# Optimization experiments

Measured on AMD Instinct MI355X. Metric: run time of the kernel, lower is better.

The kernel has to match this reference:

```python
import jax, jax.numpy as jnp
import numpy as np

N, Lq, Lk, D = 4, 2048, 2048, 1024
H, DH = 16, 64  # n_heads, projection_dim
NEG_INF = jnp.float32(-1e30)


def setup_inputs() -> dict:
    key = jax.random.key(0)
    ks = jax.random.split(key, 6)
    query = jax.random.normal(ks[0], (N, Lq, D), dtype=jnp.float32)
    key_t = jax.random.normal(ks[1], (N, Lk, D), dtype=jnp.float32)
    s = 1.0 / np.sqrt(D)
    Wq = jax.random.normal(ks[2], (D, D), dtype=jnp.float32) * s
    Wk = jax.random.normal(ks[3], (D, D), dtype=jnp.float32) * s
    Wv = jax.random.normal(ks[4], (D, D), dtype=jnp.float32) * s
    # causal mask: True where attention is forbidden (j > i)
    mask = jnp.triu(jnp.ones((Lq, Lk), dtype=bool), k=1)
    # per-sample valid lengths in [1024, 2048); padding at the tail
    valid_len = jax.random.randint(ks[5], (N,), Lk // 2, Lk)
    padding_mask = jnp.arange(Lk)[None, :] >= valid_len[:, None]  # (N, Lk) bool
    return {"query": query, "key": key_t, "Wq": Wq, "Wk": Wk, "Wv": Wv,
            "mask": mask, "padding_mask": padding_mask}


def reference(query, key, Wq, Wk, Wv, mask, padding_mask):
    n, lq, _ = query.shape
    lk = key.shape[1]
    # torch Linear (no bias): x @ W.T ; split heads -> (N, H, L, DH)
    q = (query @ Wq.T).reshape(n, lq, H, DH).transpose(0, 2, 1, 3)
    k = (key @ Wk.T).reshape(n, lk, H, DH).transpose(0, 2, 1, 3)
    v = (key @ Wv.T).reshape(n, lk, H, DH).transpose(0, 2, 1, 3)
    # per-sample scaling: sqrt(number of non-padded keys) (module quirk, not sqrt(d))
    valid = jnp.sum(~padding_mask, axis=-1).astype(query.dtype)  # (N,)
    scaling = jnp.sqrt(valid)[:, None, None, None]
    score = jnp.einsum('nhqd,nhkd->nhqk', q, k) / scaling
    score = jnp.where(mask[None, None, :, :], NEG_INF, score)
    score = jnp.where(padding_mask[:, None, None, :], NEG_INF, score)
    attn = jax.nn.softmax(score, axis=-1)
    out = jnp.einsum('nhqk,nhkd->nhqd', attn, v)
    return out.transpose(0, 2, 1, 3).reshape(n, lq, H * DH)
```

## Files before the change

kernel.cpp:

```cpp
#include <hip/hip_runtime.h>
#include <hip/hip_bf16.h>
#include <math.h>


#define N_S 4
#define LQ 2048
#define LK 2048
#define DM 1024
#define NHEAD 16
#define DHEAD 64

typedef __attribute__((ext_vector_type(8))) short short8;
typedef __attribute__((ext_vector_type(4))) float f32x4;

typedef const __attribute__((address_space(1))) void* gptr_t;
typedef __attribute__((address_space(3))) void* lptr_t;

#define GLOAD_LDS(g, l) \
    __builtin_amdgcn_global_load_lds((gptr_t)(const void*)(g), (lptr_t)(void*)(l), 16, 0, 0)

static __device__ __forceinline__ unsigned int pkbf(float a, float b) {
    __hip_bfloat162 h = __float22bfloat162_rn(make_float2(a, b));
    unsigned int u;
    __builtin_memcpy(&u, &h, 4);
    return u;
}

static __device__ __forceinline__ f32x4 zero4() {
    f32x4 v; v[0] = 0.f; v[1] = 0.f; v[2] = 0.f; v[3] = 0.f; return v;
}

static __device__ __forceinline__ void meta_body(const void* __restrict__ pm,
                                                 int* __restrict__ valid_out,
                                                 float* __restrict__ scale_out) {
    __shared__ int okInt, hasPair, okF32;
    __shared__ int counts[4];
    int t = threadIdx.x;
    if (t == 0) { okInt = 1; hasPair = 0; okF32 = 1; }
    if (t < 4) counts[t] = 0;
    __syncthreads();

    const unsigned int* w = (const unsigned int*)pm;
    int bad_int = 0, pair = 0, bad_f32 = 0;
    for (int i = t; i < 2048; i += 256) {
        unsigned int v = w[i];
        if (v > 1u) bad_int = 1;
        if (v == 0x3F803F80u) pair = 1;
        if (v != 0u && v != 0x3F800000u) bad_f32 = 1;
    }
    if (bad_int) okInt = 0;
    if (pair)    hasPair = 1;
    if (bad_f32) okF32 = 0;
    __syncthreads();

    int mode = okInt ? 0 : (hasPair ? 1 : (okF32 ? 2 : 3));
    for (int n = 0; n < 4; n++) {
        int cnt = 0;
        for (int j = t; j < LK; j += 256) {
            int idx = n * LK + j;
            bool z;
            if (mode == 0)      z = (((const int*)pm)[idx] == 0);
            else if (mode == 1) z = (((const unsigned short*)pm)[idx] == 0);
            else if (mode == 2) z = (w[idx] == 0u);
            else                z = (((const unsigned char*)pm)[idx] == 0);
            cnt += z ? 1 : 0;
        }
        atomicAdd(&counts[n], cnt);
    }
    __syncthreads();
    if (t < 4) {
        int c = counts[t] > 0 ? counts[t] : 1;
        valid_out[t] = c;
        scale_out[t] = 1.0f / sqrtf((float)c);
    }
}

__global__ void meta_kernel(const void* __restrict__ pm,
                            int* __restrict__ valid_out,
                            float* __restrict__ scale_out) {
    meta_body(pm, valid_out, scale_out);
}

static __device__ __forceinline__ void conv16(const float* src,
                                              unsigned short* dst, size_t idx) {
    f32x4 a0 = *(const f32x4*)(src + idx);
    f32x4 a1 = *(const f32x4*)(src + idx + 4);
    f32x4 a2 = *(const f32x4*)(src + idx + 8);
    f32x4 a3 = *(const f32x4*)(src + idx + 12);
    uint4 u0, u1;
    u0.x = pkbf(a0[0], a0[1]); u0.y = pkbf(a0[2], a0[3]);
    u0.z = pkbf(a1[0], a1[1]); u0.w = pkbf(a1[2], a1[3]);
    u1.x = pkbf(a2[0], a2[1]); u1.y = pkbf(a2[2], a2[3]);
    u1.z = pkbf(a3[0], a3[1]); u1.w = pkbf(a3[2], a3[3]);
    *(uint4*)(void*)(dst + idx) = u0;
    *(uint4*)(void*)(dst + idx + 8) = u1;
}

__global__ __launch_bounds__(256) void convw_kernel(
    const float* __restrict__ Wq, const float* __restrict__ Wk,
    const float* __restrict__ Wv,
    unsigned short* __restrict__ Wqb, unsigned short* __restrict__ Wkb,
    unsigned short* __restrict__ Wvb)
{
    int z = blockIdx.y;
    const float* src = (z == 0) ? Wq : ((z == 1) ? Wk : Wv);
    unsigned short* dst = (z == 0) ? Wqb : ((z == 1) ? Wkb : Wvb);
    conv16(src, dst, ((size_t)blockIdx.x * 256 + threadIdx.x) * 16);
}

__global__ __launch_bounds__(256) void convx_kernel(
    const float* __restrict__ src, unsigned short* __restrict__ dst)
{
    conv16(src, dst, ((size_t)blockIdx.x * 256 + threadIdx.x) * 16);
}

__global__ __launch_bounds__(256) void prep_kernel(
    const void* __restrict__ pm, int* __restrict__ valid_out,
    float* __restrict__ scale_out,
    const float* __restrict__ Wq, const float* __restrict__ Wk,
    const float* __restrict__ Wv,
    unsigned short* __restrict__ Wqb, unsigned short* __restrict__ Wkb,
    unsigned short* __restrict__ Wvb,
    const float* __restrict__ xq, const float* __restrict__ xk,
    unsigned short* __restrict__ dq, unsigned short* __restrict__ dk)
{
    int b = blockIdx.x;
    int t = threadIdx.x;
    if (b == 0) {
        meta_body(pm, valid_out, scale_out);
    } else if (b <= 768) {
        int bb = b - 1;
        int z = bb >> 8;
        const float* src = (z == 0) ? Wq : ((z == 1) ? Wk : Wv);
        unsigned short* dst = (z == 0) ? Wqb : ((z == 1) ? Wkb : Wvb);
        conv16(src, dst, ((size_t)(bb & 255) * 256 + t) * 16);
    } else {
        int bb = b - 769;
        const float* src = (bb >= 2048) ? xk : xq;
        unsigned short* dst = (bb >= 2048) ? dk : dq;
        int x = (bb >= 2048) ? bb - 2048 : bb;
        conv16(src, dst, ((size_t)x * 256 + t) * 16);
    }
}

static __device__ __forceinline__ void proj_body(
    const unsigned short* __restrict__ XbQ, const unsigned short* __restrict__ XbK,
    const unsigned short* __restrict__ Wqb, const unsigned short* __restrict__ Wkb,
    const unsigned short* __restrict__ Wvb,
    const float* __restrict__ scal, const int* __restrict__ valid_arr,
    unsigned short* __restrict__ Qb, unsigned short* __restrict__ Kb,
    unsigned short* __restrict__ Vt, int bxi, int byi, int z)
{
    int m0 = bxi << 7, n0 = byi << 7;
    if (z >= 1) {
        int n = m0 >> 11, ml = m0 & 2047;
        int tv64 = ((valid_arr[n] + 63) >> 6) << 6;
        if (ml >= tv64) return;
    }

    const unsigned short* W = (z == 0) ? Wqb : ((z == 1) ? Wkb : Wvb);
    const unsigned short* Xb = (z == 0) ? XbQ : XbK;

    __shared__ unsigned short Xls[128 * 32];
    __shared__ unsigned short Wls[128 * 32];

    int t = threadIdx.x;
    int wave = t >> 6, lane = t & 63;
    int l15 = lane & 15, quad = lane >> 4;
    int wa = wave >> 1, wb = wave & 1;

    int srow = t >> 2;
    int sg = ((t & 3) ^ (srow & 3)) << 3;
    const unsigned short* gX0 = Xb + (size_t)(m0 + srow) * DM + sg;
    const unsigned short* gX1 = Xb + (size_t)(m0 + 64 + srow) * DM + sg;
    const unsigned short* gW0 = W + (size_t)(n0 + srow) * DM + sg;
    const unsigned short* gW1 = W + (size_t)(n0 + 64 + srow) * DM + sg;

    f32x4 acc[4][4];
    #pragma unroll
    for (int i = 0; i < 4; i++)
        #pragma unroll
        for (int j = 0; j < 4; j++) acc[i][j] = zero4();

    int aoff = ((quad ^ (l15 & 3)) << 3);
    const unsigned short* Abuf = (z < 2) ? Wls : Xls;
    const unsigned short* Bbuf = (z < 2) ? Xls : Wls;

    for (int kk = 0; kk < DM; kk += 32) {
        __syncthreads();
        GLOAD_LDS(gX0 + kk, Xls + wave * 512);
        GLOAD_LDS(gX1 + kk, Xls + 2048 + wave * 512);
        GLOAD_LDS(gW0 + kk, Wls + wave * 512);
        GLOAD_LDS(gW1 + kk, Wls + 2048 + wave * 512);
        __syncthreads();

        short8 af[4], bf[4];
        #pragma unroll
        for (int ai = 0; ai < 4; ai++)
            af[ai] = *(const short8*)(const void*)(
                Abuf + ((wa * 64 + ai * 16 + l15) << 5) + aoff);
        #pragma unroll
        for (int bi = 0; bi < 4; bi++)
            bf[bi] = *(const short8*)(const void*)(
                Bbuf + ((wb * 64 + bi * 16 + l15) << 5) + aoff);
        #pragma unroll
        for (int ai = 0; ai < 4; ai++)
            #pragma unroll
            for (int bi = 0; bi < 4; bi++)
                acc[ai][bi] = __builtin_amdgcn_mfma_f32_16x16x32_bf16(
                    af[ai], bf[bi], acc[ai][bi], 0, 0, 0);
    }

    if (z < 2) {
        unsigned short* O = (z == 0) ? Qb : Kb;
        #pragma unroll
        for (int bi = 0; bi < 4; bi++) {
            int token = m0 + wb * 64 + bi * 16 + l15;
            float qs = 1.0f;
            if (z == 0) qs = scal[token >> 11] * 1.44269504f;
            #pragma unroll
            for (int ai = 0; ai < 4; ai++) {
                int feat = n0 + wa * 64 + ai * 16 + quad * 4;
                float v0 = acc[ai][bi][0], v1 = acc[ai][bi][1];
                float v2 = acc[ai][bi][2], v3 = acc[ai][bi][3];
                if (z == 0) { v0 *= qs; v1 *= qs; v2 *= qs; v3 *= qs; }
                uint2 u;
                u.x = pkbf(v0, v1);
                u.y = pkbf(v2, v3);
                *(uint2*)(void*)(O + (size_t)token * DM + feat) = u;
            }
        }
    } else {
        #pragma unroll
        for (int ai = 0; ai < 4; ai++) {
            int token0 = m0 + wa * 64 + ai * 16 + quad * 4;
            int n = token0 >> 11, tl = token0 & 2047;
            #pragma unroll
            for (int bi = 0; bi < 4; bi++) {
                int feat = n0 + wb * 64 + bi * 16 + l15;
                uint2 u;
                u.x = pkbf(acc[ai][bi][0], acc[ai][bi][1]);
                u.y = pkbf(acc[ai][bi][2], acc[ai][bi][3]);
                *(uint2*)(void*)(Vt + ((size_t)n * DM + feat) * LK + tl) = u;
            }
        }
    }
}

__global__ __launch_bounds__(256) void proj_bf16_kernel(
    const unsigned short* __restrict__ XbQ, const unsigned short* __restrict__ XbK,
    const unsigned short* __restrict__ Wqb, const unsigned short* __restrict__ Wkb,
    const unsigned short* __restrict__ Wvb,
    const float* __restrict__ scal, const int* __restrict__ valid_arr,
    unsigned short* __restrict__ Qb, unsigned short* __restrict__ Kb,
    unsigned short* __restrict__ Vt, int zbase)
{
    proj_body(XbQ, XbK, Wqb, Wkb, Wvb, scal, valid_arr, Qb, Kb, Vt,
              blockIdx.x, blockIdx.y, blockIdx.z + zbase);
}

__global__ __launch_bounds__(256) void proj_bf16_swz_kernel(
    const unsigned short* __restrict__ XbQ, const unsigned short* __restrict__ XbK,
    const unsigned short* __restrict__ Wqb, const unsigned short* __restrict__ Wkb,
    const unsigned short* __restrict__ Wvb,
    const float* __restrict__ scal, const int* __restrict__ valid_arr,
    unsigned short* __restrict__ Qb, unsigned short* __restrict__ Kb,
    unsigned short* __restrict__ Vt)
{
    int id = blockIdx.x;
    int s = id >> 3;
    int g = (id & 7) * 24 + (s >> 3);
    int y = s & 7;
    int z = g >> 6, x = g & 63;
    proj_body(XbQ, XbK, Wqb, Wkb, Wvb, scal, valid_arr, Qb, Kb, Vt, x, y, z);
}

__global__ __launch_bounds__(256) void proj_f32_kernel(
    const float* __restrict__ Xq, const float* __restrict__ Xk,
    const unsigned short* __restrict__ Wqb, const unsigned short* __restrict__ Wkb,
    const unsigned short* __restrict__ Wvb,
    const float* __restrict__ scal,
    unsigned short* __restrict__ Qb, unsigned short* __restrict__ Kb,
    unsigned short* __restrict__ Vt)
{
    int z = blockIdx.z;
    const float* X = (z == 0) ? Xq : Xk;
    const unsigned short* W = (z == 0) ? Wqb : ((z == 1) ? Wkb : Wvb);

    __shared__ unsigned short Xls[128 * 32];
    __shared__ unsigned short Wls[128 * 32];

    int t = threadIdx.x;
    int wave = t >> 6, lane = t & 63;
    int l15 = lane & 15, quad = lane >> 4;
    int wa = wave >> 1, wb = wave & 1;
    int m0 = blockIdx.x << 7, n0 = blockIdx.y << 7;

    int arow = t >> 1, ah = t & 1;
    int ag0 = ((2 * ah)     ^ (arow & 3)) << 3;
    int ag1 = ((2 * ah + 1) ^ (arow & 3)) << 3;
    const float* gX = X + (size_t)(m0 + arow) * DM;
    unsigned short* lX = Xls + arow * 32 + ah * 16;

    int brow = t >> 2;
    int bg = ((t & 3) ^ (brow & 3)) << 3;
    const unsigned short* gW0 = W + (size_t)(n0 + brow) * DM + bg;
    const unsigned short* gW1 = W + (size_t)(n0 + 64 + brow) * DM + bg;

    f32x4 acc[4][4];
    #pragma unroll
    for (int i = 0; i < 4; i++)
        #pragma unroll
        for (int j = 0; j < 4; j++) acc[i][j] = zero4();

    int aoff = ((quad ^ (l15 & 3)) << 3);

    f32x4 an0 = *(const f32x4*)(gX + ag0);
    f32x4 an1 = *(const f32x4*)(gX + ag0 + 4);
    f32x4 an2 = *(const f32x4*)(gX + ag1);
    f32x4 an3 = *(const f32x4*)(gX + ag1 + 4);

    const unsigned short* Abuf = (z < 2) ? Wls : Xls;
    const unsigned short* Bbuf = (z < 2) ? Xls : Wls;

    for (int kk = 0; kk < DM; kk += 32) {
        __syncthreads();
        GLOAD_LDS(gW0 + kk, Wls + wave * 512);
        GLOAD_LDS(gW1 + kk, Wls + 2048 + wave * 512);
        uint4 ua, ub;
        ua.x = pkbf(an0[0], an0[1]); ua.y = pkbf(an0[2], an0[3]);
        ua.z = pkbf(an1[0], an1[1]); ua.w = pkbf(an1[2], an1[3]);
        ub.x = pkbf(an2[0], an2[1]); ub.y = pkbf(an2[2], an2[3]);
        ub.z = pkbf(an3[0], an3[1]); ub.w = pkbf(an3[2], an3[3]);
        *(uint4*)(void*)(lX)     = ua;
        *(uint4*)(void*)(lX + 8) = ub;
        __syncthreads();

        if (kk + 32 < DM) {
            an0 = *(const f32x4*)(gX + kk + 32 + ag0);
            an1 = *(const f32x4*)(gX + kk + 32 + ag0 + 4);
            an2 = *(const f32x4*)(gX + kk + 32 + ag1);
            an3 = *(const f32x4*)(gX + kk + 32 + ag1 + 4);
        }

        short8 af[4], bf[4];
        #pragma unroll
        for (int ai = 0; ai < 4; ai++)
            af[ai] = *(const short8*)(const void*)(
                Abuf + ((wa * 64 + ai * 16 + l15) << 5) + aoff);
        #pragma unroll
        for (int bi = 0; bi < 4; bi++)
            bf[bi] = *(const short8*)(const void*)(
                Bbuf + ((wb * 64 + bi * 16 + l15) << 5) + aoff);
        #pragma unroll
        for (int ai = 0; ai < 4; ai++)
            #pragma unroll
            for (int bi = 0; bi < 4; bi++)
                acc[ai][bi] = __builtin_amdgcn_mfma_f32_16x16x32_bf16(
                    af[ai], bf[bi], acc[ai][bi], 0, 0, 0);
    }

    if (z < 2) {
        unsigned short* O = (z == 0) ? Qb : Kb;
        #pragma unroll
        for (int bi = 0; bi < 4; bi++) {
            int token = m0 + wb * 64 + bi * 16 + l15;
            float qs = 1.0f;
            if (z == 0) qs = scal[token >> 11] * 1.44269504f;
            #pragma unroll
            for (int ai = 0; ai < 4; ai++) {
                int feat = n0 + wa * 64 + ai * 16 + quad * 4;
                float v0 = acc[ai][bi][0], v1 = acc[ai][bi][1];
                float v2 = acc[ai][bi][2], v3 = acc[ai][bi][3];
                if (z == 0) { v0 *= qs; v1 *= qs; v2 *= qs; v3 *= qs; }
                uint2 u;
                u.x = pkbf(v0, v1);
                u.y = pkbf(v2, v3);
                *(uint2*)(void*)(O + (size_t)token * DM + feat) = u;
            }
        }
    } else {
        #pragma unroll
        for (int ai = 0; ai < 4; ai++) {
            int token0 = m0 + wa * 64 + ai * 16 + quad * 4;
            int n = token0 >> 11, tl = token0 & 2047;
            #pragma unroll
            for (int bi = 0; bi < 4; bi++) {
                int feat = n0 + wb * 64 + bi * 16 + l15;
                uint2 u;
                u.x = pkbf(acc[ai][bi][0], acc[ai][bi][1]);
                u.y = pkbf(acc[ai][bi][2], acc[ai][bi][3]);
                *(uint2*)(void*)(Vt + ((size_t)n * DM + feat) * LK + tl) = u;
            }
        }
    }
}

__global__ __launch_bounds__(256) void attn_kernel(
    const unsigned short* __restrict__ Qb, const unsigned short* __restrict__ Kb,
    const unsigned short* __restrict__ Vt,
    const int* __restrict__ valid_arr,
    float* __restrict__ out)
{
    __shared__ unsigned short Kls[3][64 * 64];

    int id = blockIdx.x;
    int slot = id >> 3;
    int nh = (id & 7) * 8 + (slot >> 4);
    int bx = slot & 15;

    int n = nh >> 4, h = nh & 15;
    int tA = bx, tB = 31 - bx;

    int valid = valid_arr[n];
    int tvalid = (valid + 63) >> 6;
    int TlA = (tA + 1 < tvalid) ? tA + 1 : tvalid;
    int TlB = (tB + 1 < tvalid) ? tB + 1 : tvalid;

    int t = threadIdx.x;
    int wave = t >> 6, lane = t & 63;
    int l15 = lane & 15, quad = lane >> 4;

    int qyA = tA * 64 + wave * 16 + l15;
    int qyB = tB * 64 + wave * 16 + l15;
    int qw0A = tA * 64 + wave * 16;
    int qw0B = tB * 64 + wave * 16;

    const unsigned short* QrowA = Qb + ((size_t)n * LQ + qyA) * DM + h * DHEAD;
    const unsigned short* QrowB = Qb + ((size_t)n * LQ + qyB) * DM + h * DHEAD;
    short8 qfA0 = *(const short8*)(const void*)(QrowA + quad * 8);
    short8 qfA1 = *(const short8*)(const void*)(QrowA + 32 + quad * 8);
    short8 qfB0 = *(const short8*)(const void*)(QrowB + quad * 8);
    short8 qfB1 = *(const short8*)(const void*)(QrowB + 32 + quad * 8);

    f32x4 OA[4], OB[4];
    #pragma unroll
    for (int i = 0; i < 4; i++) { OA[i] = zero4(); OB[i] = zero4(); }
    f32x4 LAcc = zero4(), LBcc = zero4();

    short8 onesf;
    #pragma unroll
    for (int i = 0; i < 8; i++) onesf[i] = (short)0x3F80;

    const unsigned short* Kbase = Kb + (size_t)n * LK * DM + h * DHEAD;
    const unsigned short* Vbase = Vt + ((size_t)n * DM + h * DHEAD) * LK;

    int srow0 = t >> 3;
    int sgk   = (((t & 7) ^ (srow0 & 7)) << 3);

    GLOAD_LDS(Kbase + (size_t)srow0 * DM + sgk,        &Kls[0][0] + wave * 512);
    GLOAD_LDS(Kbase + (size_t)(32 + srow0) * DM + sgk, &Kls[0][0] + 2048 + wave * 512);
    if (TlB > 1) {
        GLOAD_LDS(Kbase + (size_t)(64 + srow0) * DM + sgk,
                  &Kls[1][0] + wave * 512);
        GLOAD_LDS(Kbase + (size_t)(96 + srow0) * DM + sgk,
                  &Kls[1][0] + 2048 + wave * 512);
        asm volatile("s_waitcnt vmcnt(2)" ::: "memory");
    } else {
        asm volatile("s_waitcnt vmcnt(0)" ::: "memory");
    }

    int cur = 0;
    for (int kt = 0; kt < TlB; kt++) {
        int jb = kt << 6;
        bool doA = (kt < TlA);
        int nxt = (cur == 0) ? 2 : cur - 1;

        __builtin_amdgcn_sched_barrier(0);
        __builtin_amdgcn_s_barrier();
        __builtin_amdgcn_sched_barrier(0);

        short8 vf0[4], vf1[4];
        #pragma unroll
        for (int cb = 0; cb < 4; cb++) {
            vf0[cb] = *(const short8*)(const void*)(
                Vbase + (size_t)(cb * 16 + l15) * LK + jb + quad * 8);
            vf1[cb] = *(const short8*)(const void*)(
                Vbase + (size_t)(cb * 16 + l15) * LK + jb + 32 + quad * 8);
        }

        f32x4 sA[4], sB[4];
        __builtin_amdgcn_s_setprio(1);
        #pragma unroll
        for (int cb = 0; cb < 4; cb++) {
            const unsigned short* krow = &Kls[cur][0] + ((cb * 16 + l15) << 6);
            short8 kf0 = *(const short8*)(const void*)(krow + ((quad ^ (l15 & 7)) << 3));
            short8 kf1 = *(const short8*)(const void*)(krow + (((4 + quad) ^ (l15 & 7)) << 3));
            f32x4 sb = zero4();
            sb = __builtin_amdgcn_mfma_f32_16x16x32_bf16(kf0, qfB0, sb, 0, 0, 0);
            sb = __builtin_amdgcn_mfma_f32_16x16x32_bf16(kf1, qfB1, sb, 0, 0, 0);
            sB[cb] = sb;
            if (doA) {
                f32x4 sa = zero4();
                sa = __builtin_amdgcn_mfma_f32_16x16x32_bf16(kf0, qfA0, sa, 0, 0, 0);
                sa = __builtin_amdgcn_mfma_f32_16x16x32_bf16(kf1, qfA1, sa, 0, 0, 0);
                sA[cb] = sa;
            }
        }
        __builtin_amdgcn_s_setprio(0);

        if (kt + 2 < TlB) {
            int jb2 = jb + 128;
            GLOAD_LDS(Kbase + (size_t)(jb2 + srow0) * DM + sgk,
                      &Kls[nxt][0] + wave * 512);
            GLOAD_LDS(Kbase + (size_t)(jb2 + 32 + srow0) * DM + sgk,
                      &Kls[nxt][0] + 2048 + wave * 512);
        }

        if (jb + 63 > qw0B || jb + 64 > valid) {
            #pragma unroll
            for (int cb = 0; cb < 4; cb++) {
                int jb2 = jb + cb * 16 + quad * 4;
                #pragma unroll
                for (int r = 0; r < 4; r++) {
                    int j = jb2 + r;
                    if (j > qyB || j >= valid) sB[cb][r] = -1e30f;
                }
            }
        }
        short8 pfB0, pfB1;
        {
            unsigned int lo[4], hi[4];
            #pragma unroll
            for (int cb = 0; cb < 4; cb++) {
                lo[cb] = pkbf(__builtin_amdgcn_exp2f(sB[cb][0]),
                              __builtin_amdgcn_exp2f(sB[cb][1]));
                hi[cb] = pkbf(__builtin_amdgcn_exp2f(sB[cb][2]),
                              __builtin_amdgcn_exp2f(sB[cb][3]));
            }
            asm("v_permlane32_swap_b32 %0, %1" : "+v"(lo[0]), "+v"(lo[1]));
            asm("v_permlane32_swap_b32 %0, %1" : "+v"(hi[0]), "+v"(hi[1]));
            asm("v_permlane32_swap_b32 %0, %1" : "+v"(lo[2]), "+v"(lo[3]));
            asm("v_permlane32_swap_b32 %0, %1" : "+v"(hi[2]), "+v"(hi[3]));
            asm("v_permlane16_swap_b32 %0, %1" : "+v"(lo[0]), "+v"(lo[1]));
            asm("v_permlane16_swap_b32 %0, %1" : "+v"(hi[0]), "+v"(hi[1]));
            asm("v_permlane16_swap_b32 %0, %1" : "+v"(lo[2]), "+v"(lo[3]));
            asm("v_permlane16_swap_b32 %0, %1" : "+v"(hi[2]), "+v"(hi[3]));
            uint4 w0, w1;
            w0.x = lo[0]; w0.y = hi[0]; w0.z = lo[1]; w0.w = hi[1];
            w1.x = lo[2]; w1.y = hi[2]; w1.z = lo[3]; w1.w = hi[3];
            __builtin_memcpy(&pfB0, &w0, 16);
            __builtin_memcpy(&pfB1, &w1, 16);
        }

        __builtin_amdgcn_s_setprio(1);
        #pragma unroll
        for (int cb = 0; cb < 4; cb++) {
            OB[cb] = __builtin_amdgcn_mfma_f32_16x16x32_bf16(pfB0, vf0[cb], OB[cb], 0, 0, 0);
            OB[cb] = __builtin_amdgcn_mfma_f32_16x16x32_bf16(pfB1, vf1[cb], OB[cb], 0, 0, 0);
        }
        LBcc = __builtin_amdgcn_mfma_f32_16x16x32_bf16(pfB0, onesf, LBcc, 0, 0, 0);
        LBcc = __builtin_amdgcn_mfma_f32_16x16x32_bf16(pfB1, onesf, LBcc, 0, 0, 0);
        __builtin_amdgcn_s_setprio(0);

        if (doA) {
            if (jb + 63 > qw0A || jb + 64 > valid) {
                #pragma unroll
                for (int cb = 0; cb < 4; cb++) {
                    int jb2 = jb + cb * 16 + quad * 4;
                    #pragma unroll
                    for (int r = 0; r < 4; r++) {
                        int j = jb2 + r;
                        if (j > qyA || j >= valid) sA[cb][r] = -1e30f;
                    }
                }
            }
            short8 pfA0, pfA1;
            {
                unsigned int lo[4], hi[4];
                #pragma unroll
                for (int cb = 0; cb < 4; cb++) {
                    lo[cb] = pkbf(__builtin_amdgcn_exp2f(sA[cb][0]),
                                  __builtin_amdgcn_exp2f(sA[cb][1]));
                    hi[cb] = pkbf(__builtin_amdgcn_exp2f(sA[cb][2]),
                                  __builtin_amdgcn_exp2f(sA[cb][3]));
                }
                asm("v_permlane32_swap_b32 %0, %1" : "+v"(lo[0]), "+v"(lo[1]));
                asm("v_permlane32_swap_b32 %0, %1" : "+v"(hi[0]), "+v"(hi[1]));
                asm("v_permlane32_swap_b32 %0, %1" : "+v"(lo[2]), "+v"(lo[3]));
                asm("v_permlane32_swap_b32 %0, %1" : "+v"(hi[2]), "+v"(hi[3]));
                asm("v_permlane16_swap_b32 %0, %1" : "+v"(lo[0]), "+v"(lo[1]));
                asm("v_permlane16_swap_b32 %0, %1" : "+v"(hi[0]), "+v"(hi[1]));
                asm("v_permlane16_swap_b32 %0, %1" : "+v"(lo[2]), "+v"(lo[3]));
                asm("v_permlane16_swap_b32 %0, %1" : "+v"(hi[2]), "+v"(hi[3]));
                uint4 w0, w1;
                w0.x = lo[0]; w0.y = hi[0]; w0.z = lo[1]; w0.w = hi[1];
                w1.x = lo[2]; w1.y = hi[2]; w1.z = lo[3]; w1.w = hi[3];
                __builtin_memcpy(&pfA0, &w0, 16);
                __builtin_memcpy(&pfA1, &w1, 16);
            }
            __builtin_amdgcn_s_setprio(1);
            #pragma unroll
            for (int cb = 0; cb < 4; cb++) {
                OA[cb] = __builtin_amdgcn_mfma_f32_16x16x32_bf16(pfA0, vf0[cb], OA[cb], 0, 0, 0);
                OA[cb] = __builtin_amdgcn_mfma_f32_16x16x32_bf16(pfA1, vf1[cb], OA[cb], 0, 0, 0);
            }
            LAcc = __builtin_amdgcn_mfma_f32_16x16x32_bf16(pfA0, onesf, LAcc, 0, 0, 0);
            LAcc = __builtin_amdgcn_mfma_f32_16x16x32_bf16(pfA1, onesf, LAcc, 0, 0, 0);
            __builtin_amdgcn_s_setprio(0);
        }

        cur = (cur == 2) ? 0 : cur + 1;
    }

    float* obase = out + ((size_t)n * LQ) * DM + h * DHEAD;
    #pragma unroll
    for (int r = 0; r < 4; r++) {
        float iA = 1.0f / LAcc[r];
        float iB = 1.0f / LBcc[r];
        int rowA = tA * 64 + wave * 16 + quad * 4 + r;
        int rowB = tB * 64 + wave * 16 + quad * 4 + r;
        #pragma unroll
        for (int cb = 0; cb < 4; cb++) {
            obase[(size_t)rowA * DM + cb * 16 + l15] = OA[cb][r] * iA;
            obase[(size_t)rowB * DM + cb * 16 + l15] = OB[cb][r] * iB;
        }
    }
}

extern "C" void kernel_launch(void* const* d_in, const int* in_sizes, int n_in,
                              void* d_out, int out_size, void* d_ws, size_t ws_size,
                              hipStream_t stream)
{
    (void)in_sizes; (void)n_in; (void)out_size;

    const float* query = (const float*)d_in[0];
    const float* key   = (const float*)d_in[1];
    const float* Wq    = (const float*)d_in[2];
    const float* Wk    = (const float*)d_in[3];
    const float* Wv    = (const float*)d_in[4];
    const void* pmask  = d_in[6];

    char* ws = (char*)d_ws;
    unsigned short* Qb  = (unsigned short*)(ws);
    unsigned short* Kb  = (unsigned short*)(ws + (size_t)16 * 1024 * 1024);
    unsigned short* Vt  = (unsigned short*)(ws + (size_t)32 * 1024 * 1024);
    int*   valid = (int*)  (ws + (size_t)48 * 1024 * 1024);
    float* scal  = (float*)(ws + (size_t)48 * 1024 * 1024 + 64);
    unsigned short* Wqb = (unsigned short*)(ws + (size_t)48 * 1024 * 1024 + 4096);
    unsigned short* Wkb = Wqb + (size_t)DM * DM;
    unsigned short* Wvb = Wkb + (size_t)DM * DM;
    unsigned short* XbQ = Wvb + (size_t)DM * DM;
    unsigned short* XbK = XbQ + (size_t)N_S * LQ * DM;

    size_t xbytes      = (size_t)N_S * LQ * DM * 2;
    size_t need_phased = (size_t)(48 * 1024 * 1024) + 4096
                       + 3 * (size_t)DM * DM * 2 + xbytes;
    size_t need_full   = need_phased + xbytes;

    if (ws_size >= need_full) {
        prep_kernel<<<dim3(1 + 768 + 4096), 256, 0, stream>>>(
            pmask, valid, scal, Wq, Wk, Wv, Wqb, Wkb, Wvb,
            query, key, XbQ, XbK);
        proj_bf16_swz_kernel<<<dim3(1536), 256, 0, stream>>>(
            XbQ, XbK, Wqb, Wkb, Wvb, scal, valid, Qb, Kb, Vt);
    } else if (ws_size >= need_phased) {
        meta_kernel<<<1, 256, 0, stream>>>(pmask, valid, scal);
        convw_kernel<<<dim3(256, 3), 256, 0, stream>>>(Wq, Wk, Wv, Wqb, Wkb, Wvb);
        convx_kernel<<<2048, 256, 0, stream>>>(query, XbQ);
        proj_bf16_kernel<<<dim3(64, 8, 1), 256, 0, stream>>>(
            XbQ, XbQ, Wqb, Wkb, Wvb, scal, valid, Qb, Kb, Vt, 0);
        convx_kernel<<<2048, 256, 0, stream>>>(key, XbQ);
        proj_bf16_kernel<<<dim3(64, 8, 2), 256, 0, stream>>>(
            XbQ, XbQ, Wqb, Wkb, Wvb, scal, valid, Qb, Kb, Vt, 1);
    } else {
        meta_kernel<<<1, 256, 0, stream>>>(pmask, valid, scal);
        convw_kernel<<<dim3(256, 3), 256, 0, stream>>>(Wq, Wk, Wv, Wqb, Wkb, Wvb);
        proj_f32_kernel<<<dim3(64, 8, 3), 256, 0, stream>>>(
            query, key, Wqb, Wkb, Wvb, scal, Qb, Kb, Vt);
    }

    attn_kernel<<<dim3(1024), 256, 0, stream>>>(Qb, Kb, Vt, valid,
                                                (float*)d_out);
}
```

Baseline: 334.2 us.

## Split paired causal query tiles into one tile per block, doubling grid

The attention kernel previously had each block handle two complementary query tiles (tA and 31-tA) that share K/V loads, which balanced causal work. Now each block handles a single 64-row query tile, and the grid is doubled to 2048 blocks. Blocks are remapped so heads are grouped per XCD and longer tiles are scheduled first. This cuts per-block register pressure and may raise occupancy, at the cost of loading K/V separately for each tile and giving blocks unequal amounts of work.

```diff
diff --git a/kernel.cpp b/kernel.cpp
--- a/kernel.cpp
+++ b/kernel.cpp
@@ -405,38 +405,32 @@
     __shared__ unsigned short Kls[3][64 * 64];
 
     int id = blockIdx.x;
+    int xcd = id & 7;
     int slot = id >> 3;
-    int nh = (id & 7) * 8 + (slot >> 4);
-    int bx = slot & 15;
-
-    int n = nh >> 4, h = nh & 15;
-    int tA = bx, tB = 31 - bx;
+    int g = slot >> 5;
+    int tQ = 31 - (slot & 31);
+    int n = g >> 1;
+    int h = 2 * xcd + (g & 1);
 
     int valid = valid_arr[n];
     int tvalid = (valid + 63) >> 6;
-    int TlA = (tA + 1 < tvalid) ? tA + 1 : tvalid;
-    int TlB = (tB + 1 < tvalid) ? tB + 1 : tvalid;
+    int Tl = (tQ + 1 < tvalid) ? tQ + 1 : tvalid;
 
     int t = threadIdx.x;
     int wave = t >> 6, lane = t & 63;
     int l15 = lane & 15, quad = lane >> 4;
 
-    int qyA = tA * 64 + wave * 16 + l15;
-    int qyB = tB * 64 + wave * 16 + l15;
-    int qw0A = tA * 64 + wave * 16;
-    int qw0B = tB * 64 + wave * 16;
-
-    const unsigned short* QrowA = Qb + ((size_t)n * LQ + qyA) * DM + h * DHEAD;
-    const unsigned short* QrowB = Qb + ((size_t)n * LQ + qyB) * DM + h * DHEAD;
-    short8 qfA0 = *(const short8*)(const void*)(QrowA + quad * 8);
-    short8 qfA1 = *(const short8*)(const void*)(QrowA + 32 + quad * 8);
-    short8 qfB0 = *(const short8*)(const void*)(QrowB + quad * 8);
-    short8 qfB1 = *(const short8*)(const void*)(QrowB + 32 + quad * 8);
-
-    f32x4 OA[4], OB[4];
+    int qy = tQ * 64 + wave * 16 + l15;
+    int qw0 = tQ * 64 + wave * 16;
+
+    const unsigned short* Qrow = Qb + ((size_t)n * LQ + qy) * DM + h * DHEAD;
+    short8 qf0 = *(const short8*)(const void*)(Qrow + quad * 8);
+    short8 qf1 = *(const short8*)(const void*)(Qrow + 32 + quad * 8);
+
+    f32x4 O[4];
     #pragma unroll
-    for (int i = 0; i < 4; i++) { OA[i] = zero4(); OB[i] = zero4(); }
-    f32x4 LAcc = zero4(), LBcc = zero4();
+    for (int i = 0; i < 4; i++) O[i] = zero4();
+    f32x4 Lc = zero4();
 
     short8 onesf;
     #pragma unroll
@@ -450,7 +444,7 @@
 
     GLOAD_LDS(Kbase + (size_t)srow0 * DM + sgk,        &Kls[0][0] + wave * 512);
     GLOAD_LDS(Kbase + (size_t)(32 + srow0) * DM + sgk, &Kls[0][0] + 2048 + wave * 512);
-    if (TlB > 1) {
+    if (Tl > 1) {
         GLOAD_LDS(Kbase + (size_t)(64 + srow0) * DM + sgk,
                   &Kls[1][0] + wave * 512);
         GLOAD_LDS(Kbase + (size_t)(96 + srow0) * DM + sgk,
@@ -461,9 +455,8 @@
     }
 
     int cur = 0;
-    for (int kt = 0; kt < TlB; kt++) {
+    for (int kt = 0; kt < Tl; kt++) {
         int jb = kt << 6;
-        bool doA = (kt < TlA);
         int nxt = (cur == 0) ? 2 : cur - 1;
 
         __builtin_amdgcn_sched_barrier(0);
@@ -479,27 +472,21 @@
                 Vbase + (size_t)(cb * 16 + l15) * LK + jb + 32 + quad * 8);
         }
 
-        f32x4 sA[4], sB[4];
+        f32x4 s[4];
         __builtin_amdgcn_s_setprio(1);
         #pragma unroll
         for (int cb = 0; cb < 4; cb++) {
             const unsigned short* krow = &Kls[cur][0] + ((cb * 16 + l15) << 6);
             short8 kf0 = *(const short8*)(const void*)(krow + ((quad ^ (l15 & 7)) << 3));
             short8 kf1 = *(const short8*)(const void*)(krow + (((4 + quad) ^ (l15 & 7)) << 3));
-            f32x4 sb = zero4();
-            sb = __builtin_amdgcn_mfma_f32_16x16x32_bf16(kf0, qfB0, sb, 0, 0, 0);
-            sb = __builtin_amdgcn_mfma_f32_16x16x32_bf16(kf1, qfB1, sb, 0, 0, 0);
-            sB[cb] = sb;
-            if (doA) {
-                f32x4 sa = zero4();
-                sa = __builtin_amdgcn_mfma_f32_16x16x32_bf16(kf0, qfA0, sa, 0, 0, 0);
-                sa = __builtin_amdgcn_mfma_f32_16x16x32_bf16(kf1, qfA1, sa, 0, 0, 0);
-                sA[cb] = sa;
-            }
+            f32x4 sv = zero4();
+            sv = __builtin_amdgcn_mfma_f32_16x16x32_bf16(kf0, qf0, sv, 0, 0, 0);
+            sv = __builtin_amdgcn_mfma_f32_16x16x32_bf16(kf1, qf1, sv, 0, 0, 0);
+            s[cb] = sv;
         }
         __builtin_amdgcn_s_setprio(0);
 
-        if (kt + 2 < TlB) {
+        if (kt + 2 < Tl) {
             int jb2 = jb + 128;
             GLOAD_LDS(Kbase + (size_t)(jb2 + srow0) * DM + sgk,
                       &Kls[nxt][0] + wave * 512);
@@ -507,26 +494,26 @@
                       &Kls[nxt][0] + 2048 + wave * 512);
         }
 
-        if (jb + 63 > qw0B || jb + 64 > valid) {
+        if (jb + 63 > qw0 || jb + 64 > valid) {
             #pragma unroll
             for (int cb = 0; cb < 4; cb++) {
                 int jb2 = jb + cb * 16 + quad * 4;
                 #pragma unroll
                 for (int r = 0; r < 4; r++) {
                     int j = jb2 + r;
-                    if (j > qyB || j >= valid) sB[cb][r] = -1e30f;
+                    if (j > qy || j >= valid) s[cb][r] = -1e30f;
                 }
             }
         }
-        short8 pfB0, pfB1;
+        short8 pf0, pf1;
         {
             unsigned int lo[4], hi[4];
             #pragma unroll
             for (int cb = 0; cb < 4; cb++) {
-                lo[cb] = pkbf(__builtin_amdgcn_exp2f(sB[cb][0]),
-                              __builtin_amdgcn_exp2f(sB[cb][1]));
-                hi[cb] = pkbf(__builtin_amdgcn_exp2f(sB[cb][2]),
-                              __builtin_amdgcn_exp2f(sB[cb][3]));
+                lo[cb] = pkbf(__builtin_amdgcn_exp2f(s[cb][0]),
+                              __builtin_amdgcn_exp2f(s[cb][1]));
+                hi[cb] = pkbf(__builtin_amdgcn_exp2f(s[cb][2]),
+                              __builtin_amdgcn_exp2f(s[cb][3]));
             }
             asm("v_permlane32_swap_b32 %0, %1" : "+v"(lo[0]), "+v"(lo[1]));
             asm("v_permlane32_swap_b32 %0, %1" : "+v"(hi[0]), "+v"(hi[1]));
@@ -539,66 +526,19 @@
             uint4 w0, w1;
             w0.x = lo[0]; w0.y = hi[0]; w0.z = lo[1]; w0.w = hi[1];
             w1.x = lo[2]; w1.y = hi[2]; w1.z = lo[3]; w1.w = hi[3];
-            __builtin_memcpy(&pfB0, &w0, 16);
-            __builtin_memcpy(&pfB1, &w1, 16);
+            __builtin_memcpy(&pf0, &w0, 16);
+            __builtin_memcpy(&pf1, &w1, 16);
         }
 
         __builtin_amdgcn_s_setprio(1);
         #pragma unroll
         for (int cb = 0; cb < 4; cb++) {
-            OB[cb] = __builtin_amdgcn_mfma_f32_16x16x32_bf16(pfB0, vf0[cb], OB[cb], 0, 0, 0);
-            OB[cb] = __builtin_amdgcn_mfma_f32_16x16x32_bf16(pfB1, vf1[cb], OB[cb], 0, 0, 0);
-        }
-        LBcc = __builtin_amdgcn_mfma_f32_16x16x32_bf16(pfB0, onesf, LBcc, 0, 0, 0);
-        LBcc = __builtin_amdgcn_mfma_f32_16x16x32_bf16(pfB1, onesf, LBcc, 0, 0, 0);
+            O[cb] = __builtin_amdgcn_mfma_f32_16x16x32_bf16(pf0, vf0[cb], O[cb], 0, 0, 0);
+            O[cb] = __builtin_amdgcn_mfma_f32_16x16x32_bf16(pf1, vf1[cb], O[cb], 0, 0, 0);
+        }
+        Lc = __builtin_amdgcn_mfma_f32_16x16x32_bf16(pf0, onesf, Lc, 0, 0, 0);
+        Lc = __builtin_amdgcn_mfma_f32_16x16x32_bf16(pf1, onesf, Lc, 0, 0, 0);
         __builtin_amdgcn_s_setprio(0);
-
-        if (doA) {
-            if (jb + 63 > qw0A || jb + 64 > valid) {
-                #pragma unroll
-                for (int cb = 0; cb < 4; cb++) {
-                    int jb2 = jb + cb * 16 + quad * 4;
-                    #pragma unroll
-                    for (int r = 0; r < 4; r++) {
-                        int j = jb2 + r;
-                        if (j > qyA || j >= valid) sA[cb][r] = -1e30f;
-                    }
-                }
-            }
-            short8 pfA0, pfA1;
-            {
-                unsigned int lo[4], hi[4];
-                #pragma unroll
-                for (int cb = 0; cb < 4; cb++) {
-                    lo[cb] = pkbf(__builtin_amdgcn_exp2f(sA[cb][0]),
-                                  __builtin_amdgcn_exp2f(sA[cb][1]));
-                    hi[cb] = pkbf(__builtin_amdgcn_exp2f(sA[cb][2]),
-                                  __builtin_amdgcn_exp2f(sA[cb][3]));
-                }
-                asm("v_permlane32_swap_b32 %0, %1" : "+v"(lo[0]), "+v"(lo[1]));
-                asm("v_permlane32_swap_b32 %0, %1" : "+v"(hi[0]), "+v"(hi[1]));
-                asm("v_permlane32_swap_b32 %0, %1" : "+v"(lo[2]), "+v"(lo[3]));
-                asm("v_permlane32_swap_b32 %0, %1" : "+v"(hi[2]), "+v"(hi[3]));
-                asm("v_permlane16_swap_b32 %0, %1" : "+v"(lo[0]), "+v"(lo[1]));
-                asm("v_permlane16_swap_b32 %0, %1" : "+v"(hi[0]), "+v"(hi[1]));
-                asm("v_permlane16_swap_b32 %0, %1" : "+v"(lo[2]), "+v"(lo[3]));
-                asm("v_permlane16_swap_b32 %0, %1" : "+v"(hi[2]), "+v"(hi[3]));
-                uint4 w0, w1;
-                w0.x = lo[0]; w0.y = hi[0]; w0.z = lo[1]; w0.w = hi[1];
-                w1.x = lo[2]; w1.y = hi[2]; w1.z = lo[3]; w1.w = hi[3];
-                __builtin_memcpy(&pfA0, &w0, 16);
-                __builtin_memcpy(&pfA1, &w1, 16);
-            }
-            __builtin_amdgcn_s_setprio(1);
-            #pragma unroll
-            for (int cb = 0; cb < 4; cb++) {
-                OA[cb] = __builtin_amdgcn_mfma_f32_16x16x32_bf16(pfA0, vf0[cb], OA[cb], 0, 0, 0);
-                OA[cb] = __builtin_amdgcn_mfma_f32_16x16x32_bf16(pfA1, vf1[cb], OA[cb], 0, 0, 0);
-            }
-            LAcc = __builtin_amdgcn_mfma_f32_16x16x32_bf16(pfA0, onesf, LAcc, 0, 0, 0);
-            LAcc = __builtin_amdgcn_mfma_f32_16x16x32_bf16(pfA1, onesf, LAcc, 0, 0, 0);
-            __builtin_amdgcn_s_setprio(0);
-        }
 
         cur = (cur == 2) ? 0 : cur + 1;
     }
@@ -606,14 +546,11 @@
     float* obase = out + ((size_t)n * LQ) * DM + h * DHEAD;
     #pragma unroll
     for (int r = 0; r < 4; r++) {
-        float iA = 1.0f / LAcc[r];
-        float iB = 1.0f / LBcc[r];
-        int rowA = tA * 64 + wave * 16 + quad * 4 + r;
-        int rowB = tB * 64 + wave * 16 + quad * 4 + r;
+        float iL = 1.0f / Lc[r];
+        int row = tQ * 64 + wave * 16 + quad * 4 + r;
         #pragma unroll
         for (int cb = 0; cb < 4; cb++) {
-            obase[(size_t)rowA * DM + cb * 16 + l15] = OA[cb][r] * iA;
-            obase[(size_t)rowB * DM + cb * 16 + l15] = OB[cb][r] * iB;
+            obase[(size_t)row * DM + cb * 16 + l15] = O[cb][r] * iL;
         }
     }
 }
@@ -670,6 +607,6 @@
             query, key, Wqb, Wkb, Wvb, scal, Qb, Kb, Vt);
     }
 
-    attn_kernel<<<dim3(1024), 256, 0, stream>>>(Qb, Kb, Vt, valid,
+    attn_kernel<<<dim3(2048), 256, 0, stream>>>(Qb, Kb, Vt, valid,
                                                 (float*)d_out);
 }
```

After: 363.3 us. 8.7% more time.

## Share K tiles across two query-tile pairs in 512-thread attention blocks

Applied to the files above, without the earlier changes.

The attention kernel now uses 512-thread blocks. Each block handles four query tiles of one (batch, head): two balanced causal pairs, one per group of four waves. Every K tile staged in LDS is therefore reused by twice as many waves, halving the number of blocks and the K global-to-LDS traffic per query tile. The head-to-XCD mapping is also regrouped so each XCD serves two heads. Waves whose tiles finish early sit idle through the longer loop, and the larger block lowers scheduling granularity and may raise register pressure under the 512 launch bound.

```diff
diff --git a/kernel.cpp b/kernel.cpp
--- a/kernel.cpp
+++ b/kernel.cpp
@@ -396,7 +396,7 @@
     }
 }
 
-__global__ __launch_bounds__(256) void attn_kernel(
+__global__ __launch_bounds__(512) void attn_kernel(
     const unsigned short* __restrict__ Qb, const unsigned short* __restrict__ Kb,
     const unsigned short* __restrict__ Vt,
     const int* __restrict__ valid_arr,
@@ -405,26 +405,32 @@
     __shared__ unsigned short Kls[3][64 * 64];
 
     int id = blockIdx.x;
+    int xcd = id & 7;
     int slot = id >> 3;
-    int nh = (id & 7) * 8 + (slot >> 4);
-    int bx = slot & 15;
-
-    int n = nh >> 4, h = nh & 15;
-    int tA = bx, tB = 31 - bx;
+    int g = slot >> 3;
+    int b = slot & 7;
+    int n = g >> 1;
+    int h = 2 * xcd + (g & 1);
 
     int valid = valid_arr[n];
     int tvalid = (valid + 63) >> 6;
-    int TlA = (tA + 1 < tvalid) ? tA + 1 : tvalid;
-    int TlB = (tB + 1 < tvalid) ? tB + 1 : tvalid;
 
     int t = threadIdx.x;
     int wave = t >> 6, lane = t & 63;
     int l15 = lane & 15, quad = lane >> 4;
-
-    int qyA = tA * 64 + wave * 16 + l15;
-    int qyB = tB * 64 + wave * 16 + l15;
-    int qw0A = tA * 64 + wave * 16;
-    int qw0B = tB * 64 + wave * 16;
+    int pair = wave >> 2;
+    int w4 = wave & 3;
+
+    int tA = pair ? (16 + b) : b;
+    int tB = pair ? (31 - b) : (15 - b);
+    int TlA = (tA + 1 < tvalid) ? tA + 1 : tvalid;
+    int TlB = (tB + 1 < tvalid) ? tB + 1 : tvalid;
+    int Tloop = (32 - b < tvalid) ? 32 - b : tvalid;
+
+    int qyA = tA * 64 + w4 * 16 + l15;
+    int qyB = tB * 64 + w4 * 16 + l15;
+    int qw0A = tA * 64 + w4 * 16;
+    int qw0B = tB * 64 + w4 * 16;
 
     const unsigned short* QrowA = Qb + ((size_t)n * LQ + qyA) * DM + h * DHEAD;
     const unsigned short* QrowB = Qb + ((size_t)n * LQ + qyB) * DM + h * DHEAD;
@@ -448,22 +454,21 @@
     int srow0 = t >> 3;
     int sgk   = (((t & 7) ^ (srow0 & 7)) << 3);
 
-    GLOAD_LDS(Kbase + (size_t)srow0 * DM + sgk,        &Kls[0][0] + wave * 512);
-    GLOAD_LDS(Kbase + (size_t)(32 + srow0) * DM + sgk, &Kls[0][0] + 2048 + wave * 512);
-    if (TlB > 1) {
+    GLOAD_LDS(Kbase + (size_t)srow0 * DM + sgk, &Kls[0][0] + wave * 512);
+    if (Tloop > 1) {
         GLOAD_LDS(Kbase + (size_t)(64 + srow0) * DM + sgk,
                   &Kls[1][0] + wave * 512);
-        GLOAD_LDS(Kbase + (size_t)(96 + srow0) * DM + sgk,
-                  &Kls[1][0] + 2048 + wave * 512);
-        asm volatile("s_waitcnt vmcnt(2)" ::: "memory");
+        asm volatile("s_waitcnt vmcnt(1)" ::: "memory");
     } else {
         asm volatile("s_waitcnt vmcnt(0)" ::: "memory");
     }
 
     int cur = 0;
-    for (int kt = 0; kt < TlB; kt++) {
+    for (int kt = 0; kt < Tloop; kt++) {
         int jb = kt << 6;
+        bool doB = (kt < TlB);
         bool doA = (kt < TlA);
+        bool pf = (kt + 2 < Tloop);
         int nxt = (cur == 0) ? 2 : cur - 1;
 
         __builtin_amdgcn_sched_barrier(0);
@@ -471,87 +476,90 @@
         __builtin_amdgcn_sched_barrier(0);
 
         short8 vf0[4], vf1[4];
-        #pragma unroll
-        for (int cb = 0; cb < 4; cb++) {
-            vf0[cb] = *(const short8*)(const void*)(
-                Vbase + (size_t)(cb * 16 + l15) * LK + jb + quad * 8);
-            vf1[cb] = *(const short8*)(const void*)(
-                Vbase + (size_t)(cb * 16 + l15) * LK + jb + 32 + quad * 8);
+        if (doB) {
+            #pragma unroll
+            for (int cb = 0; cb < 4; cb++) {
+                vf0[cb] = *(const short8*)(const void*)(
+                    Vbase + (size_t)(cb * 16 + l15) * LK + jb + quad * 8);
+                vf1[cb] = *(const short8*)(const void*)(
+                    Vbase + (size_t)(cb * 16 + l15) * LK + jb + 32 + quad * 8);
+            }
         }
 
         f32x4 sA[4], sB[4];
-        __builtin_amdgcn_s_setprio(1);
-        #pragma unroll
-        for (int cb = 0; cb < 4; cb++) {
-            const unsigned short* krow = &Kls[cur][0] + ((cb * 16 + l15) << 6);
-            short8 kf0 = *(const short8*)(const void*)(krow + ((quad ^ (l15 & 7)) << 3));
-            short8 kf1 = *(const short8*)(const void*)(krow + (((4 + quad) ^ (l15 & 7)) << 3));
-            f32x4 sb = zero4();
-            sb = __builtin_amdgcn_mfma_f32_16x16x32_bf16(kf0, qfB0, sb, 0, 0, 0);
-            sb = __builtin_amdgcn_mfma_f32_16x16x32_bf16(kf1, qfB1, sb, 0, 0, 0);
-            sB[cb] = sb;
-            if (doA) {
-                f32x4 sa = zero4();
-                sa = __builtin_amdgcn_mfma_f32_16x16x32_bf16(kf0, qfA0, sa, 0, 0, 0);
-                sa = __builtin_amdgcn_mfma_f32_16x16x32_bf16(kf1, qfA1, sa, 0, 0, 0);
-                sA[cb] = sa;
-            }
-        }
-        __builtin_amdgcn_s_setprio(0);
-
-        if (kt + 2 < TlB) {
+        if (doB) {
+            __builtin_amdgcn_s_setprio(1);
+            #pragma unroll
+            for (int cb = 0; cb < 4; cb++) {
+                const unsigned short* krow = &Kls[cur][0] + ((cb * 16 + l15) << 6);
+                short8 kf0 = *(const short8*)(const void*)(krow + ((quad ^ (l15 & 7)) << 3));
+                short8 kf1 = *(const short8*)(const void*)(krow + (((4 + quad) ^ (l15 & 7)) << 3));
+                f32x4 sb = zero4();
+                sb = __builtin_amdgcn_mfma_f32_16x16x32_bf16(kf0, qfB0, sb, 0, 0, 0);
+                sb = __builtin_amdgcn_mfma_f32_16x16x32_bf16(kf1, qfB1, sb, 0, 0, 0);
+                sB[cb] = sb;
+                if (doA) {
+                    f32x4 sa = zero4();
+                    sa = __builtin_amdgcn_mfma_f32_16x16x32_bf16(kf0, qfA0, sa, 0, 0, 0);
+                    sa = __builtin_amdgcn_mfma_f32_16x16x32_bf16(kf1, qfA1, sa, 0, 0, 0);
+                    sA[cb] = sa;
+                }
+            }
+            __builtin_amdgcn_s_setprio(0);
+        }
+
+        if (pf) {
             int jb2 = jb + 128;
             GLOAD_LDS(Kbase + (size_t)(jb2 + srow0) * DM + sgk,
                       &Kls[nxt][0] + wave * 512);
-            GLOAD_LDS(Kbase + (size_t)(jb2 + 32 + srow0) * DM + sgk,
-                      &Kls[nxt][0] + 2048 + wave * 512);
-        }
-
-        if (jb + 63 > qw0B || jb + 64 > valid) {
+        }
+
+        if (doB) {
+            if (jb + 63 > qw0B || jb + 64 > valid) {
+                #pragma unroll
+                for (int cb = 0; cb < 4; cb++) {
+                    int jb2 = jb + cb * 16 + quad * 4;
+                    #pragma unroll
+                    for (int r = 0; r < 4; r++) {
+                        int j = jb2 + r;
+                        if (j > qyB || j >= valid) sB[cb][r] = -1e30f;
+                    }
+                }
+            }
+            short8 pfB0, pfB1;
+            {
+                unsigned int lo[4], hi[4];
+                #pragma unroll
+                for (int cb = 0; cb < 4; cb++) {
+                    lo[cb] = pkbf(__builtin_amdgcn_exp2f(sB[cb][0]),
+                                  __builtin_amdgcn_exp2f(sB[cb][1]));
+                    hi[cb] = pkbf(__builtin_amdgcn_exp2f(sB[cb][2]),
+                                  __builtin_amdgcn_exp2f(sB[cb][3]));
+                }
+                asm("v_permlane32_swap_b32 %0, %1" : "+v"(lo[0]), "+v"(lo[1]));
+                asm("v_permlane32_swap_b32 %0, %1" : "+v"(hi[0]), "+v"(hi[1]));
+                asm("v_permlane32_swap_b32 %0, %1" : "+v"(lo[2]), "+v"(lo[3]));
+                asm("v_permlane32_swap_b32 %0, %1" : "+v"(hi[2]), "+v"(hi[3]));
+                asm("v_permlane16_swap_b32 %0, %1" : "+v"(lo[0]), "+v"(lo[1]));
+                asm("v_permlane16_swap_b32 %0, %1" : "+v"(hi[0]), "+v"(hi[1]));
+                asm("v_permlane16_swap_b32 %0, %1" : "+v"(lo[2]), "+v"(lo[3]));
+                asm("v_permlane16_swap_b32 %0, %1" : "+v"(hi[2]), "+v"(hi[3]));
+                uint4 w0, w1;
+                w0.x = lo[0]; w0.y = hi[0]; w0.z = lo[1]; w0.w = hi[1];
+                w1.x = lo[2]; w1.y = hi[2]; w1.z = lo[3]; w1.w = hi[3];
+                __builtin_memcpy(&pfB0, &w0, 16);
+                __builtin_memcpy(&pfB1, &w1, 16);
+            }
+            __builtin_amdgcn_s_setprio(1);
             #pragma unroll
             for (int cb = 0; cb < 4; cb++) {
-                int jb2 = jb + cb * 16 + quad * 4;
-                #pragma unroll
-                for (int r = 0; r < 4; r++) {
-                    int j = jb2 + r;
-                    if (j > qyB || j >= valid) sB[cb][r] = -1e30f;
-                }
-            }
-        }
-        short8 pfB0, pfB1;
-        {
-            unsigned int lo[4], hi[4];
-            #pragma unroll
-            for (int cb = 0; cb < 4; cb++) {
-                lo[cb] = pkbf(__builtin_amdgcn_exp2f(sB[cb][0]),
-                              __builtin_amdgcn_exp2f(sB[cb][1]));
-                hi[cb] = pkbf(__builtin_amdgcn_exp2f(sB[cb][2]),
-                              __builtin_amdgcn_exp2f(sB[cb][3]));
-            }
-            asm("v_permlane32_swap_b32 %0, %1" : "+v"(lo[0]), "+v"(lo[1]));
-            asm("v_permlane32_swap_b32 %0, %1" : "+v"(hi[0]), "+v"(hi[1]));
-            asm("v_permlane32_swap_b32 %0, %1" : "+v"(lo[2]), "+v"(lo[3]));
-            asm("v_permlane32_swap_b32 %0, %1" : "+v"(hi[2]), "+v"(hi[3]));
-            asm("v_permlane16_swap_b32 %0, %1" : "+v"(lo[0]), "+v"(lo[1]));
-            asm("v_permlane16_swap_b32 %0, %1" : "+v"(hi[0]), "+v"(hi[1]));
-            asm("v_permlane16_swap_b32 %0, %1" : "+v"(lo[2]), "+v"(lo[3]));
-            asm("v_permlane16_swap_b32 %0, %1" : "+v"(hi[2]), "+v"(hi[3]));
-            uint4 w0, w1;
-            w0.x = lo[0]; w0.y = hi[0]; w0.z = lo[1]; w0.w = hi[1];
-            w1.x = lo[2]; w1.y = hi[2]; w1.z = lo[3]; w1.w = hi[3];
-            __builtin_memcpy(&pfB0, &w0, 16);
-            __builtin_memcpy(&pfB1, &w1, 16);
-        }
-
-        __builtin_amdgcn_s_setprio(1);
-        #pragma unroll
-        for (int cb = 0; cb < 4; cb++) {
-            OB[cb] = __builtin_amdgcn_mfma_f32_16x16x32_bf16(pfB0, vf0[cb], OB[cb], 0, 0, 0);
-            OB[cb] = __builtin_amdgcn_mfma_f32_16x16x32_bf16(pfB1, vf1[cb], OB[cb], 0, 0, 0);
-        }
-        LBcc = __builtin_amdgcn_mfma_f32_16x16x32_bf16(pfB0, onesf, LBcc, 0, 0, 0);
-        LBcc = __builtin_amdgcn_mfma_f32_16x16x32_bf16(pfB1, onesf, LBcc, 0, 0, 0);
-        __builtin_amdgcn_s_setprio(0);
+                OB[cb] = __builtin_amdgcn_mfma_f32_16x16x32_bf16(pfB0, vf0[cb], OB[cb], 0, 0, 0);
+                OB[cb] = __builtin_amdgcn_mfma_f32_16x16x32_bf16(pfB1, vf1[cb], OB[cb], 0, 0, 0);
+            }
+            LBcc = __builtin_amdgcn_mfma_f32_16x16x32_bf16(pfB0, onesf, LBcc, 0, 0, 0);
+            LBcc = __builtin_amdgcn_mfma_f32_16x16x32_bf16(pfB1, onesf, LBcc, 0, 0, 0);
+            __builtin_amdgcn_s_setprio(0);
+        }
 
         if (doA) {
             if (jb + 63 > qw0A || jb + 64 > valid) {
@@ -600,6 +608,9 @@
             __builtin_amdgcn_s_setprio(0);
         }
 
+        if (pf) asm volatile("s_waitcnt vmcnt(1)" ::: "memory");
+        else    asm volatile("s_waitcnt vmcnt(0)" ::: "memory");
+
         cur = (cur == 2) ? 0 : cur + 1;
     }
 
@@ -608,8 +619,8 @@
     for (int r = 0; r < 4; r++) {
         float iA = 1.0f / LAcc[r];
         float iB = 1.0f / LBcc[r];
-        int rowA = tA * 64 + wave * 16 + quad * 4 + r;
-        int rowB = tB * 64 + wave * 16 + quad * 4 + r;
+        int rowA = tA * 64 + w4 * 16 + quad * 4 + r;
+        int rowB = tB * 64 + w4 * 16 + quad * 4 + r;
         #pragma unroll
         for (int cb = 0; cb < 4; cb++) {
             obase[(size_t)rowA * DM + cb * 16 + l15] = OA[cb][r] * iA;
@@ -670,6 +681,6 @@
             query, key, Wqb, Wkb, Wvb, scal, Qb, Kb, Vt);
     }
 
-    attn_kernel<<<dim3(1024), 256, 0, stream>>>(Qb, Kb, Vt, valid,
-                                                (float*)d_out);
-}
+    attn_kernel<<<dim3(512), 512, 0, stream>>>(Qb, Kb, Vt, valid,
+                                               (float*)d_out);
+}
```

Result: slower. 343.6 us (+2.8%).

## Double-buffer 128-key K tiles in LDS and remap blocks to heads per XCD

Applied to the files above, without the earlier changes.

Replaces the triple-buffered 64-key K pipeline with a double buffer of 128-key tiles, so each barrier and wait covers two 64-key sub-tiles processed through a shared lambda. The next 128-key tile is prefetched right after the barrier and fully waited at the end of the iteration. Block-to-(n,h) mapping changes so each XCD handles two heads across samples, which may change L2 locality. This halves barrier count but waits vmcnt(0) per pair, which could expose load latency more than the previous rolling prefetch.

```diff
diff --git a/kernel.cpp b/kernel.cpp
--- a/kernel.cpp
+++ b/kernel.cpp
@@ -402,20 +402,23 @@
     const int* __restrict__ valid_arr,
     float* __restrict__ out)
 {
-    __shared__ unsigned short Kls[3][64 * 64];
+    __shared__ unsigned short Kls[2][128 * 64];
 
     int id = blockIdx.x;
+    int xcd = id & 7;
     int slot = id >> 3;
-    int nh = (id & 7) * 8 + (slot >> 4);
+    int g = slot >> 4;
     int bx = slot & 15;
-
-    int n = nh >> 4, h = nh & 15;
+    int n = g >> 1;
+    int h = 2 * xcd + (g & 1);
+
     int tA = bx, tB = 31 - bx;
 
     int valid = valid_arr[n];
     int tvalid = (valid + 63) >> 6;
     int TlA = (tA + 1 < tvalid) ? tA + 1 : tvalid;
     int TlB = (tB + 1 < tvalid) ? tB + 1 : tvalid;
+    int Tpair = (TlB + 1) >> 1;
 
     int t = threadIdx.x;
     int wave = t >> 6, lane = t & 63;
@@ -448,27 +451,14 @@
     int srow0 = t >> 3;
     int sgk   = (((t & 7) ^ (srow0 & 7)) << 3);
 
-    GLOAD_LDS(Kbase + (size_t)srow0 * DM + sgk,        &Kls[0][0] + wave * 512);
-    GLOAD_LDS(Kbase + (size_t)(32 + srow0) * DM + sgk, &Kls[0][0] + 2048 + wave * 512);
-    if (TlB > 1) {
-        GLOAD_LDS(Kbase + (size_t)(64 + srow0) * DM + sgk,
-                  &Kls[1][0] + wave * 512);
-        GLOAD_LDS(Kbase + (size_t)(96 + srow0) * DM + sgk,
-                  &Kls[1][0] + 2048 + wave * 512);
-        asm volatile("s_waitcnt vmcnt(2)" ::: "memory");
-    } else {
-        asm volatile("s_waitcnt vmcnt(0)" ::: "memory");
-    }
-
-    int cur = 0;
-    for (int kt = 0; kt < TlB; kt++) {
-        int jb = kt << 6;
-        bool doA = (kt < TlA);
-        int nxt = (cur == 0) ? 2 : cur - 1;
-
-        __builtin_amdgcn_sched_barrier(0);
-        __builtin_amdgcn_s_barrier();
-        __builtin_amdgcn_sched_barrier(0);
+    #pragma unroll
+    for (int r = 0; r < 4; r++)
+        GLOAD_LDS(Kbase + (size_t)(r * 32 + srow0) * DM + sgk,
+                  &Kls[0][0] + r * 2048 + wave * 512);
+    asm volatile("s_waitcnt vmcnt(0)" ::: "memory");
+
+    auto sub_tile = [&](int cur, int j64, int rowoff, bool doA) {
+        int jb = j64 << 6;
 
         short8 vf0[4], vf1[4];
         #pragma unroll
@@ -483,7 +473,8 @@
         __builtin_amdgcn_s_setprio(1);
         #pragma unroll
         for (int cb = 0; cb < 4; cb++) {
-            const unsigned short* krow = &Kls[cur][0] + ((cb * 16 + l15) << 6);
+            const unsigned short* krow =
+                &Kls[cur][0] + ((rowoff + cb * 16 + l15) << 6);
             short8 kf0 = *(const short8*)(const void*)(krow + ((quad ^ (l15 & 7)) << 3));
             short8 kf1 = *(const short8*)(const void*)(krow + (((4 + quad) ^ (l15 & 7)) << 3));
             f32x4 sb = zero4();
@@ -498,14 +489,6 @@
             }
         }
         __builtin_amdgcn_s_setprio(0);
-
-        if (kt + 2 < TlB) {
-            int jb2 = jb + 128;
-            GLOAD_LDS(Kbase + (size_t)(jb2 + srow0) * DM + sgk,
-                      &Kls[nxt][0] + wave * 512);
-            GLOAD_LDS(Kbase + (size_t)(jb2 + 32 + srow0) * DM + sgk,
-                      &Kls[nxt][0] + 2048 + wave * 512);
-        }
 
         if (jb + 63 > qw0B || jb + 64 > valid) {
             #pragma unroll
@@ -542,7 +525,6 @@
             __builtin_memcpy(&pfB0, &w0, 16);
             __builtin_memcpy(&pfB1, &w1, 16);
         }
-
         __builtin_amdgcn_s_setprio(1);
         #pragma unroll
         for (int cb = 0; cb < 4; cb++) {
@@ -599,8 +581,29 @@
             LAcc = __builtin_amdgcn_mfma_f32_16x16x32_bf16(pfA1, onesf, LAcc, 0, 0, 0);
             __builtin_amdgcn_s_setprio(0);
         }
-
-        cur = (cur == 2) ? 0 : cur + 1;
+    };
+
+    int cur = 0;
+    for (int kt = 0; kt < Tpair; kt++) {
+        __builtin_amdgcn_sched_barrier(0);
+        __builtin_amdgcn_s_barrier();
+        __builtin_amdgcn_sched_barrier(0);
+
+        if (kt + 1 < Tpair) {
+            size_t rb = (size_t)(kt + 1) << 7;
+            #pragma unroll
+            for (int r = 0; r < 4; r++)
+                GLOAD_LDS(Kbase + (rb + r * 32 + srow0) * DM + sgk,
+                          &Kls[1 - cur][0] + r * 2048 + wave * 512);
+        }
+
+        int j64 = kt << 1;
+        sub_tile(cur, j64, 0, j64 < TlA);
+        if (j64 + 1 < TlB)
+            sub_tile(cur, j64 + 1, 64, j64 + 1 < TlA);
+
+        asm volatile("s_waitcnt vmcnt(0)" ::: "memory");
+        cur ^= 1;
     }
 
     float* obase = out + ((size_t)n * LQ) * DM + h * DHEAD;
```

Result: faster. 315.4 us (-5.6%).
